# Optimization experiments

Measured on AMD Instinct MI355X. Metric: run time of the kernel, lower is better.

Reference implementation:

```python
import jax, jax.numpy as jnp
from jax import lax
import numpy as np

C = 256       # residual_channels == skip_channels
B = 4
T = 4096
LATENT = 128
NB = 4        # n_blocks
NL = 10       # n_layers
ENC_DILS = tuple(2 ** i for i in range(NL)) * NB   # 40 encoder blocks
DEC_DILS = tuple(2 ** i for i in range(NL))        # 10 decoder blocks


def causal_conv(x, W, b, d):
    # x: [B, Cin, T], W: [Cout, Cin, k], left-pad by (k-1)*d for causality
    pad = (W.shape[-1] - 1) * d
    y = lax.conv_general_dilated(x, W, (1,), [(pad, 0)], rhs_dilation=(d,),
                                 dimension_numbers=('NCH', 'OIH', 'NCH'))
    return y + b[None, :, None]


def gated_block(h, Wf, bf, Wg, bg, Wr, br, Ws, bs, d):
    f = jnp.tanh(causal_conv(h, Wf, bf, d))
    g = jax.nn.sigmoid(causal_conv(h, Wg, bg, d))
    out = f * g
    res = jnp.einsum('oc,bct->bot', Wr, out) + br[None, :, None] + h
    skip = jnp.einsum('oc,bct->bot', Ws, out) + bs[None, :, None]
    return res, skip


def setup_inputs() -> dict:
    key = jax.random.key(0)
    ks = jax.random.split(key, 24)
    s = 0.05
    nE = NB * NL
    d = {}
    d['x'] = jax.random.normal(ks[0], (B, 1, T), jnp.float32)
    d['eps'] = jax.random.normal(ks[1], (B, LATENT), jnp.float32)
    d['enc_in_W'] = jax.random.normal(ks[2], (C, 1, 2)) * s
    d['enc_in_b'] = jnp.zeros((C,), jnp.float32)
    d['enc_Wf'] = jax.random.normal(ks[3], (nE, C, C, 2)) * s
    d['enc_bf'] = jnp.zeros((nE, C), jnp.float32)
    d['enc_Wg'] = jax.random.normal(ks[4], (nE, C, C, 2)) * s
    d['enc_bg'] = jnp.zeros((nE, C), jnp.float32)
    d['enc_Wr'] = jax.random.normal(ks[5], (nE, C, C)) * s
    d['enc_br'] = jnp.zeros((nE, C), jnp.float32)
    d['enc_Ws'] = jax.random.normal(ks[6], (nE, C, C)) * s
    d['enc_bs'] = jnp.zeros((nE, C), jnp.float32)
    d['fc_mu_W'] = jax.random.normal(ks[7], (LATENT, C)) * s
    d['fc_mu_b'] = jnp.zeros((LATENT,), jnp.float32)
    d['fc_lv_W'] = jax.random.normal(ks[8], (LATENT, C)) * s
    d['fc_lv_b'] = jnp.zeros((LATENT,), jnp.float32)
    d['dec_in_W'] = jax.random.normal(ks[9], (C, LATENT)) * s
    d['dec_in_b'] = jnp.zeros((C,), jnp.float32)
    d['dec_Wf'] = jax.random.normal(ks[10], (NL, C, C, 2)) * s
    d['dec_bf'] = jnp.zeros((NL, C), jnp.float32)
    d['dec_Wg'] = jax.random.normal(ks[11], (NL, C, C, 2)) * s
    d['dec_bg'] = jnp.zeros((NL, C), jnp.float32)
    d['dec_Wr'] = jax.random.normal(ks[12], (NL, C, C)) * s
    d['dec_br'] = jnp.zeros((NL, C), jnp.float32)
    d['out_W'] = jax.random.normal(ks[13], (1, C)) * s
    d['out_b'] = jnp.zeros((1,), jnp.float32)
    return d


def _forward(x, eps, enc_in_W, enc_in_b, enc_Wf, enc_bf, enc_Wg, enc_bg,
             enc_Wr, enc_br, enc_Ws, enc_bs, fc_mu_W, fc_mu_b, fc_lv_W, fc_lv_b,
             dec_in_W, dec_in_b, dec_Wf, dec_bf, dec_Wg, dec_bg, dec_Wr, dec_br,
             out_W, out_b):
    # --- encode ---
    h = causal_conv(x, enc_in_W, enc_in_b, 1)
    skip_sum = jnp.zeros((h.shape[0], C, h.shape[2]), h.dtype)
    for i, dil in enumerate(ENC_DILS):
        h, skip = gated_block(h, enc_Wf[i], enc_bf[i], enc_Wg[i], enc_bg[i],
                              enc_Wr[i], enc_br[i], enc_Ws[i], enc_bs[i], dil)
        skip_sum = skip_sum + skip
    pooled = skip_sum.mean(axis=-1)                      # [B, C]
    mu = pooled @ fc_mu_W.T + fc_mu_b                    # [B, LATENT]
    logvar = pooled @ fc_lv_W.T + fc_lv_b
    # --- reparameterize ---
    z = mu + eps * jnp.exp(0.5 * logvar)
    # --- decode (length-1 sequence) ---
    h2 = (jnp.einsum('ol,bl->bo', dec_in_W, z) + dec_in_b)[:, :, None]  # [B, C, 1]
    for i, dil in enumerate(DEC_DILS):
        f = jnp.tanh(causal_conv(h2, dec_Wf[i], dec_bf[i], dil))
        g = jax.nn.sigmoid(causal_conv(h2, dec_Wg[i], dec_bg[i], dil))
        out = f * g
        h2 = jnp.einsum('oc,bct->bot', dec_Wr[i], out) + dec_br[i][None, :, None] + h2
    y = jnp.einsum('oc,bct->bot', out_W, h2) + out_b[None, :, None]     # [B, 1, 1]
    return (y, mu, logvar)


def reference(x, eps, enc_in_W, enc_in_b, enc_Wf, enc_bf, enc_Wg, enc_bg,
              enc_Wr, enc_br, enc_Ws, enc_bs, fc_mu_W, fc_mu_b, fc_lv_W, fc_lv_b,
              dec_in_W, dec_in_b, dec_Wf, dec_bf, dec_Wg, dec_bg, dec_Wr, dec_br,
              out_W, out_b):
    return _forward(x, eps, enc_in_W, enc_in_b, enc_Wf, enc_bf, enc_Wg, enc_bg,
                    enc_Wr, enc_br, enc_Ws, enc_bs, fc_mu_W, fc_mu_b, fc_lv_W, fc_lv_b,
                    dec_in_W, dec_in_b, dec_Wf, dec_bf, dec_Wg, dec_bg, dec_Wr, dec_br,
                    out_W, out_b)
```

## Files before the change

### kernel.cpp

```cpp
#include <hip/hip_runtime.h>

typedef unsigned short u16;
typedef __attribute__((ext_vector_type(8))) __bf16 bf16x8;
typedef __attribute__((ext_vector_type(4))) float f32x4;

constexpr int C = 256;
constexpr int T = 4096;
constexpr int B = 4;
constexpr int NENC = 40;
constexpr int NDEC = 10;
constexpr int TILE = 64;

__device__ __forceinline__ float bf2f(u16 v) {
  union { unsigned u; float f; } x;
  x.u = ((unsigned)v) << 16;
  return x.f;
}
__device__ __forceinline__ u16 f2bf(float f) {
  union { float ff; unsigned u; } x;
  x.ff = f;
  unsigned r = x.u + 0x7fffu + ((x.u >> 16) & 1u);
  return (u16)(r >> 16);
}
__device__ __forceinline__ int swz(int row, int col) {
  int g = ((row & 7) ^ (row >> 3)) & 7;
  return row * 512 + (col ^ (g << 3));
}

typedef __attribute__((address_space(1))) const unsigned int* gp1_t;
typedef __attribute__((address_space(3))) unsigned int* lp3_t;
__device__ __forceinline__ void gl_lds16(const u16* g, u16* l) {
  __builtin_amdgcn_global_load_lds((gp1_t)(const void*)g, (lp3_t)(void*)l, 16, 0, 0);
}

__global__ void k_pack1(const float* __restrict__ Wf, const float* __restrict__ Wg,
                        u16* __restrict__ penc1, int total) {
  int p = blockIdx.x * 256 + threadIdx.x;
  if (p >= total) return;
  int lane = p & 63;
  int s = (p >> 6) & 3;
  int c = (p >> 8) & 15;
  int wv = (p >> 12) & 7;
  int layer = p >> 15;
  int co = wv * 32 + (s & 1) * 16 + (lane & 15);
  int k = c * 32 + (lane >> 4) * 8;
  const float* src = (s >= 2 ? Wg : Wf) + ((size_t)layer * C + co) * 512 + k;
  u16* dst = penc1 + (size_t)p * 8;
#pragma unroll
  for (int r = 0; r < 8; ++r) dst[r] = f2bf(src[r]);
}

__global__ void k_pack2(const float* __restrict__ Wr, u16* __restrict__ penc2, int total) {
  int p = blockIdx.x * 256 + threadIdx.x;
  if (p >= total) return;
  int lane = p & 63;
  int s = (p >> 6) & 1;
  int c = (p >> 7) & 7;
  int wv = (p >> 10) & 7;
  int layer = p >> 13;
  int co = wv * 32 + s * 16 + (lane & 15);
  int k = c * 32 + (lane >> 4) * 8;
  const float* src = Wr + ((size_t)layer * C + co) * 256 + k;
  u16* dst = penc2 + (size_t)p * 8;
#pragma unroll
  for (int r = 0; r < 8; ++r) dst[r] = f2bf(src[r]);
}

__global__ void k_packd(const float* __restrict__ dWf, const float* __restrict__ dWg,
                        const float* __restrict__ dWr, const float* __restrict__ dinW,
                        u16* __restrict__ pdfg, u16* __restrict__ pdr,
                        u16* __restrict__ tdin) {
  int p = blockIdx.x * 256 + threadIdx.x;
  if (p < 163840) {
    int lane = p & 63;
    int s = (p >> 6) & 1;
    int c = (p >> 7) & 7;
    int wv = (p >> 10) & 15;
    int layer = p >> 14;
    int co = wv * 16 + (lane & 15);
    int k = c * 32 + (lane >> 4) * 8;
    const float* src = (s ? dWg : dWf) + (((size_t)(layer * C + co)) * C + k) * 2 + 1;
    u16* dst = pdfg + (size_t)p * 8;
#pragma unroll
    for (int r = 0; r < 8; ++r) dst[r] = f2bf(src[2 * r]);
  } else if (p < 245760) {
    int q = p - 163840;
    int lane = q & 63;
    int c = (q >> 6) & 7;
    int wv = (q >> 9) & 15;
    int layer = q >> 13;
    int co = wv * 16 + (lane & 15);
    int k = c * 32 + (lane >> 4) * 8;
    const float* src = dWr + ((size_t)(layer * C + co)) * C + k;
    u16* dst = pdr + (size_t)q * 8;
#pragma unroll
    for (int r = 0; r < 8; ++r) dst[r] = f2bf(src[r]);
  } else if (p < 249856) {
    int u = p - 245760;
#pragma unroll
    for (int r = 0; r < 8; ++r) tdin[u * 8 + r] = f2bf(dinW[u * 8 + r]);
  }
}

__global__ void k_zero(float* __restrict__ p, int n) {
  int i = blockIdx.x * 256 + threadIdx.x;
  if (i < n) p[i] = 0.f;
}

__global__ void k_input(const float* __restrict__ x, const float* __restrict__ W,
                        const float* __restrict__ bin, float* __restrict__ h) {
  int idx = blockIdx.x * 256 + threadIdx.x;
  int t = idx & (T - 1);
  int c = (idx >> 12) & (C - 1);
  int b = idx >> 20;
  float xv = x[b * T + t];
  float xp = (t > 0) ? x[b * T + t - 1] : 0.f;
  h[idx] = W[2 * c] * xp + W[2 * c + 1] * xv + bin[c];
}

__global__ __launch_bounds__(1024, 4) void k_enc(
    const float* __restrict__ hin, float* __restrict__ hout, float* __restrict__ rowsum_l,
    const u16* __restrict__ pw1, const float* __restrict__ bfb,
    const float* __restrict__ bgb,
    const u16* __restrict__ pw2, const float* __restrict__ brb,
    int dil) {
  extern __shared__ __align__(16) u16 smem[];
  const int tid = threadIdx.x;
  const int wave = tid >> 6;
  const int lane = tid & 63;
  const int ncol = lane & 15;
  const int quad = lane >> 4;
  const int wg = blockIdx.x;
  const int b = wg >> 6;
  const int t0 = (wg & 63) * TILE;
  const float* hb = hin + b * C * T;

  const int co0 = wave * 16;
  const int kq = quad * 8;
  const int off1 = (wg >> 3) & 15;
  const int off2 = (wg >> 3) & 7;
  const u16* b1w = pw1 + (wave >> 1) * 32768 + (wave & 1) * 512 + lane * 8;
  const u16* b2w = pw2 + (wave >> 1) * 8192 + (wave & 1) * 512 + lane * 8;

  const int n4 = tid & 15;
  const int cib = tid >> 4;
  float4 v0[4], v1[4];
  const bool al4 = ((dil & 3) == 0);
  if (t0 >= dil) {
#pragma unroll
    for (int j = 0; j < 4; ++j) {
      int ci = cib + j * 64;
      const float* p = hb + ci * T + t0 + n4 * 4 - dil;
      if (al4) {
        v0[j] = *(const float4*)p;
      } else {
        v0[j].x = p[0]; v0[j].y = p[1]; v0[j].z = p[2]; v0[j].w = p[3];
      }
      v1[j] = *(const float4*)(hb + ci * T + t0 + n4 * 4);
    }
  } else {
#pragma unroll
    for (int j = 0; j < 4; ++j) {
      int ci = cib + j * 64;
      int tb = t0 + n4 * 4 - dil;
      const float* p = hb + ci * T + tb;
      v0[j].x = (tb + 0 >= 0) ? p[0] : 0.f;
      v0[j].y = (tb + 1 >= 0) ? p[1] : 0.f;
      v0[j].z = (tb + 2 >= 0) ? p[2] : 0.f;
      v0[j].w = (tb + 3 >= 0) ? p[3] : 0.f;
      v1[j] = *(const float4*)(hb + ci * T + t0 + n4 * 4);
    }
  }
#pragma unroll
  for (int j = 0; j < 4; ++j) {
    int ci = cib + j * 64;
    const float* p0 = (const float*)&v0[j];
    const float* p1 = (const float*)&v1[j];
#pragma unroll
    for (int r = 0; r < 4; ++r) {
      unsigned w32 = (unsigned)f2bf(p0[r]) | ((unsigned)f2bf(p1[r]) << 16);
      *(unsigned*)(&smem[swz(n4 * 4 + r, 2 * ci)]) = w32;
    }
  }

  bf16x8 wf[2], wg_[2];
  {
    const u16* gs = b1w + (off1 & 15) * 2048;
    wf[0] = *(const bf16x8*)gs;
    wg_[0] = *(const bf16x8*)(gs + 1024);
  }
  __syncthreads();

  f32x4 acc[2][4];
#pragma unroll
  for (int m = 0; m < 2; ++m)
#pragma unroll
    for (int nt = 0; nt < 4; ++nt)
      acc[m][nt] = (f32x4){0.f, 0.f, 0.f, 0.f};

#pragma unroll 2
  for (int c = 0; c < 16; ++c) {
    const int cb = c & 1;
    if (c < 15) {
      const u16* gs = b1w + ((c + 1 + off1) & 15) * 2048;
      wf[cb ^ 1] = *(const bf16x8*)gs;
      wg_[cb ^ 1] = *(const bf16x8*)(gs + 1024);
    }
    const int kk = ((c + off1) & 15) * 32 + kq;
    bf16x8 bfr[4];
#pragma unroll
    for (int nt = 0; nt < 4; ++nt)
      bfr[nt] = *(const bf16x8*)(&smem[swz(nt * 16 + ncol, kk)]);
#pragma unroll
    for (int nt = 0; nt < 4; ++nt) {
      acc[0][nt] = __builtin_amdgcn_mfma_f32_16x16x32_bf16(wf[cb], bfr[nt], acc[0][nt], 0, 0, 0);
      acc[1][nt] = __builtin_amdgcn_mfma_f32_16x16x32_bf16(wg_[cb], bfr[nt], acc[1][nt], 0, 0, 0);
    }
  }

  bf16x8 w2[2];
  {
    const u16* gs = b2w + (off2 & 7) * 1024;
    w2[0] = *(const bf16x8*)gs;
  }
  __syncthreads();

  float* rsb = rowsum_l + b * C;
  {
    const int cob = co0 + quad * 4;
    float bfv[4], bgv[4], rs[4];
#pragma unroll
    for (int r = 0; r < 4; ++r) {
      bfv[r] = bfb[cob + r];
      bgv[r] = bgb[cob + r];
      rs[r] = 0.f;
    }
#pragma unroll
    for (int nt = 0; nt < 4; ++nt) {
      const int n = nt * 16 + ncol;
      u16 pk[4];
#pragma unroll
      for (int r = 0; r < 4; ++r) {
        float fv = acc[0][nt][r] + bfv[r];
        float gv = acc[1][nt][r] + bgv[r];
        float th = 1.f - 2.f / (__expf(2.f * fv) + 1.f);
        float sg = 1.f / (1.f + __expf(-gv));
        float o = th * sg;
        rs[r] += o;
        pk[r] = f2bf(o);
      }
      uint2 w;
      w.x = (unsigned)pk[0] | ((unsigned)pk[1] << 16);
      w.y = (unsigned)pk[2] | ((unsigned)pk[3] << 16);
      *(uint2*)(&smem[swz(n, cob)]) = w;
    }
#pragma unroll
    for (int r = 0; r < 4; ++r) {
      float s = rs[r];
      s += __shfl_xor(s, 1);
      s += __shfl_xor(s, 2);
      s += __shfl_xor(s, 4);
      s += __shfl_xor(s, 8);
      if (ncol == 0) atomicAdd(&rsb[cob + r], s);
    }
  }
  __syncthreads();

  f32x4 acc2[4];
#pragma unroll
  for (int nt = 0; nt < 4; ++nt)
    acc2[nt] = (f32x4){0.f, 0.f, 0.f, 0.f};

#pragma unroll 2
  for (int c = 0; c < 8; ++c) {
    const int cb = c & 1;
    if (c < 7) {
      const u16* gs = b2w + ((c + 1 + off2) & 7) * 1024;
      w2[cb ^ 1] = *(const bf16x8*)gs;
    }
    const int kk = ((c + off2) & 7) * 32 + kq;
    bf16x8 bfr[4];
#pragma unroll
    for (int nt = 0; nt < 4; ++nt)
      bfr[nt] = *(const bf16x8*)(&smem[swz(nt * 16 + ncol, kk)]);
#pragma unroll
    for (int nt = 0; nt < 4; ++nt)
      acc2[nt] = __builtin_amdgcn_mfma_f32_16x16x32_bf16(w2[cb], bfr[nt], acc2[nt], 0, 0, 0);
  }
  __syncthreads();

  float* fb = (float*)smem;
  {
    const int cob = co0 + quad * 4;
#pragma unroll
    for (int nt = 0; nt < 4; ++nt) {
      const int t = nt * 16 + ncol;
#pragma unroll
      for (int r = 0; r < 4; ++r)
        fb[(cob + r) * 66 + t] = acc2[nt][r] + brb[cob + r];
    }
  }
  __syncthreads();
  float* ho = hout + b * C * T;
#pragma unroll
  for (int j = 0; j < 4; ++j) {
    const int ci = cib + j * 64;
    const float* fr = fb + ci * 66 + n4 * 4;
    float4 o;
    o.x = fr[0] + v1[j].x;
    o.y = fr[1] + v1[j].y;
    o.z = fr[2] + v1[j].z;
    o.w = fr[3] + v1[j].w;
    *(float4*)(ho + ci * T + t0 + n4 * 4) = o;
  }
}

__global__ __launch_bounds__(256) void k_skip(
    const float* __restrict__ encWs, const float* __restrict__ encbs,
    const float* __restrict__ rowsum, float* __restrict__ pooled) {
  __shared__ float rs[B][C];
  const int l = blockIdx.x;
  const int co = threadIdx.x;
  for (int i = co; i < B * C; i += 256) rs[i >> 8][i & 255] = rowsum[l * B * C + i];
  __syncthreads();
  const float* Wrow = encWs + (size_t)l * C * C + co * C;
  float bs = encbs[l * C + co] * (float)T;
  float d[B] = {0.f, 0.f, 0.f, 0.f};
  for (int ci = 0; ci < C; ci += 4) {
    float4 w = *(const float4*)(Wrow + ci);
#pragma unroll
    for (int b = 0; b < B; ++b)
      d[b] += w.x * rs[b][ci] + w.y * rs[b][ci + 1] + w.z * rs[b][ci + 2] + w.w * rs[b][ci + 3];
  }
#pragma unroll
  for (int b = 0; b < B; ++b) atomicAdd(&pooled[b * C + co], d[b] + bs);
}

__global__ __launch_bounds__(256) void k_fc(
    const float* __restrict__ pooled,
    const float* __restrict__ muW, const float* __restrict__ mub,
    const float* __restrict__ lvW, const float* __restrict__ lvb,
    float* __restrict__ mlbuf, float* __restrict__ dout) {
  __shared__ float pm[B * C];
  const int tid = threadIdx.x;
  for (int i = tid; i < B * C; i += 256) pm[i] = pooled[i] * (1.f / (float)T);
  __syncthreads();
  const int waveG = blockIdx.x * 4 + (tid >> 6);
  const int lane = tid & 63;
  for (int j = 0; j < 16; ++j) {
    int d = waveG * 16 + j;
    int b = d >> 8, r = d & 255, which = r >> 7, l = r & 127;
    const float* Wrow = (which ? lvW : muW) + l * C;
    const float* p = pm + b * C;
    float s = Wrow[lane] * p[lane] + Wrow[lane + 64] * p[lane + 64] +
              Wrow[lane + 128] * p[lane + 128] + Wrow[lane + 192] * p[lane + 192];
#pragma unroll
    for (int off = 32; off; off >>= 1) s += __shfl_xor(s, off);
    if (lane == 0) {
      float val = s + (which ? lvb[l] : mub[l]);
      mlbuf[which * 512 + b * 128 + l] = val;
      dout[4 + which * 512 + b * 128 + l] = val;
    }
  }
}

__global__ __launch_bounds__(1024, 1) void k_dec(
    const float* __restrict__ mlbuf, const float* __restrict__ eps,
    const u16* __restrict__ tdin, const float* __restrict__ dinb,
    const u16* __restrict__ pdfg, const float* __restrict__ dbf,
    const float* __restrict__ dbg,
    const u16* __restrict__ pdr, const float* __restrict__ dbr,
    const float* __restrict__ outW, const float* __restrict__ outb,
    float* __restrict__ dout) {
  extern __shared__ __align__(16) u16 dsm[];
  __shared__ __align__(16) u16 Ah[16][264];
  __shared__ __align__(16) u16 Ao[16][264];
  __shared__ float h2f[4][256];
  __shared__ float outred[4];
  const int tid = threadIdx.x;
  const int wave = tid >> 6;
  const int lane = tid & 63;
  const int ncol = lane & 15;
  const int quad = lane >> 4;
  const int kq = quad * 8;
  const int co = wave * 16 + ncol;
  u16* wreg = dsm + wave * 4096;

  bf16x8 tdw[4];
  {
    const u16* wp = tdin + co * 128;
#pragma unroll
    for (int it = 0; it < 4; ++it) tdw[it] = *(const bf16x8*)(wp + it * 32 + kq);
  }

  if (tid < 512) {
    int b = tid >> 7, l = tid & 127;
    float mu = mlbuf[b * 128 + l];
    float lv = mlbuf[512 + b * 128 + l];
    Ah[b][l] = f2bf(mu + eps[b * 128 + l] * expf(0.5f * lv));
  }
  if (tid < 4) outred[tid] = 0.f;
  __syncthreads();

  {
    f32x4 acch = (f32x4){0.f, 0.f, 0.f, 0.f};
#pragma unroll
    for (int it = 0; it < 4; ++it) {
      bf16x8 af = *(const bf16x8*)(&Ah[ncol][it * 32 + kq]);
      acch = __builtin_amdgcn_mfma_f32_16x16x32_bf16(af, tdw[it], acch, 0, 0, 0);
    }
    __syncthreads();
    if (quad == 0) {
      float bias = dinb[co];
#pragma unroll
      for (int r = 0; r < 4; ++r) {
        float hv = acch[r] + bias;
        h2f[r][co] = hv;
        Ah[r][co] = f2bf(hv);
      }
    }
  }
  {
    const u16* fb = pdfg + wave * 8192 + lane * 8;
#pragma unroll
    for (int cc = 0; cc < 4; ++cc) {
      gl_lds16(fb + cc * 1024, wreg + cc * 1024);
      gl_lds16(fb + cc * 1024 + 512, wreg + cc * 1024 + 512);
    }
  }
  __syncthreads();

  for (int i = 0; i < NDEC; ++i) {
    const u16* fb = pdfg + (i * 16 + wave) * 8192 + lane * 8;
    const u16* rb = pdr + (i * 16 + wave) * 4096 + lane * 8;

    f32x4 accf = (f32x4){0.f, 0.f, 0.f, 0.f};
    f32x4 accg = (f32x4){0.f, 0.f, 0.f, 0.f};
#pragma unroll
    for (int c = 0; c < 8; ++c) {
      if (c == 4) asm volatile("s_waitcnt vmcnt(6)" ::: "memory");
      else if (c == 5) asm volatile("s_waitcnt vmcnt(4)" ::: "memory");
      else if (c == 6) asm volatile("s_waitcnt vmcnt(2)" ::: "memory");
      else if (c == 7) asm volatile("s_waitcnt vmcnt(0)" ::: "memory");
      const u16* bufp = wreg + (c & 3) * 1024;
      bf16x8 bf_ = *(const bf16x8*)(bufp + lane * 8);
      bf16x8 bg_ = *(const bf16x8*)(bufp + 512 + lane * 8);
      bf16x8 af = *(const bf16x8*)(&Ah[ncol][c * 32 + kq]);
      accf = __builtin_amdgcn_mfma_f32_16x16x32_bf16(af, bf_, accf, 0, 0, 0);
      accg = __builtin_amdgcn_mfma_f32_16x16x32_bf16(af, bg_, accg, 0, 0, 0);
      if (c < 4) {
        asm volatile("s_waitcnt lgkmcnt(0)" ::: "memory");
        gl_lds16(fb + (c + 4) * 1024, wreg + (c & 3) * 1024);
        gl_lds16(fb + (c + 4) * 1024 + 512, wreg + (c & 3) * 1024 + 512);
      }
    }
    asm volatile("s_waitcnt lgkmcnt(0)" ::: "memory");
#pragma unroll
    for (int cc = 0; cc < 4; ++cc) gl_lds16(rb + cc * 512, wreg + cc * 1024);

    if (quad == 0) {
      float bfv = dbf[i * C + co];
      float bgv = dbg[i * C + co];
#pragma unroll
      for (int r = 0; r < 4; ++r) {
        float fv = accf[r] + bfv;
        float gv = accg[r] + bgv;
        float th = 1.f - 2.f / (__expf(2.f * fv) + 1.f);
        float sg = 1.f / (1.f + __expf(-gv));
        Ao[r][co] = f2bf(th * sg);
      }
    }
    __syncthreads();

    f32x4 accr = (f32x4){0.f, 0.f, 0.f, 0.f};
#pragma unroll
    for (int c = 0; c < 8; ++c) {
      if (c == 4) asm volatile("s_waitcnt vmcnt(3)" ::: "memory");
      else if (c == 5) asm volatile("s_waitcnt vmcnt(2)" ::: "memory");
      else if (c == 6) asm volatile("s_waitcnt vmcnt(1)" ::: "memory");
      else if (c == 7) asm volatile("s_waitcnt vmcnt(0)" ::: "memory");
      bf16x8 br_ = *(const bf16x8*)(wreg + (c & 3) * 1024 + lane * 8);
      bf16x8 af = *(const bf16x8*)(&Ao[ncol][c * 32 + kq]);
      accr = __builtin_amdgcn_mfma_f32_16x16x32_bf16(af, br_, accr, 0, 0, 0);
      if (c < 4) {
        asm volatile("s_waitcnt lgkmcnt(0)" ::: "memory");
        gl_lds16(rb + (c + 4) * 512, wreg + (c & 3) * 1024);
      }
    }
    if (i + 1 < NDEC) {
      const u16* nfb = pdfg + ((i + 1) * 16 + wave) * 8192 + lane * 8;
      asm volatile("s_waitcnt lgkmcnt(0)" ::: "memory");
#pragma unroll
      for (int cc = 0; cc < 4; ++cc) {
        gl_lds16(nfb + cc * 1024, wreg + cc * 1024);
        gl_lds16(nfb + cc * 1024 + 512, wreg + cc * 1024 + 512);
      }
    }
    if (quad == 0) {
      float brv = dbr[i * C + co];
#pragma unroll
      for (int r = 0; r < 4; ++r) {
        float hv = h2f[r][co] + accr[r] + brv;
        h2f[r][co] = hv;
        Ah[r][co] = f2bf(hv);
      }
    }
    __syncthreads();
  }

  {
    int b = tid >> 8, c = tid & 255;
    float val = outW[c] * h2f[b][c];
#pragma unroll
    for (int off = 32; off; off >>= 1) val += __shfl_xor(val, off);
    if (lane == 0) atomicAdd(&outred[b], val);
  }
  __syncthreads();
  if (tid < 4) dout[tid] = outred[tid] + outb[0];
}

extern "C" void kernel_launch(void* const* d_in, const int* in_sizes, int n_in,
                              void* d_out, int out_size, void* d_ws, size_t ws_size,
                              hipStream_t stream) {
  const float* x      = (const float*)d_in[0];
  const float* eps    = (const float*)d_in[1];
  const float* encinW = (const float*)d_in[2];
  const float* encinb = (const float*)d_in[3];
  const float* encWf  = (const float*)d_in[4];
  const float* encbf  = (const float*)d_in[5];
  const float* encWg  = (const float*)d_in[6];
  const float* encbg  = (const float*)d_in[7];
  const float* encWr  = (const float*)d_in[8];
  const float* encbr  = (const float*)d_in[9];
  const float* encWs  = (const float*)d_in[10];
  const float* encbs  = (const float*)d_in[11];
  const float* muW    = (const float*)d_in[12];
  const float* mub    = (const float*)d_in[13];
  const float* lvW    = (const float*)d_in[14];
  const float* lvb    = (const float*)d_in[15];
  const float* dinW   = (const float*)d_in[16];
  const float* dinb   = (const float*)d_in[17];
  const float* dWf    = (const float*)d_in[18];
  const float* dbf    = (const float*)d_in[19];
  const float* dWg    = (const float*)d_in[20];
  const float* dbg    = (const float*)d_in[21];
  const float* dWr    = (const float*)d_in[22];
  const float* dbr    = (const float*)d_in[23];
  const float* outW   = (const float*)d_in[24];
  const float* outb   = (const float*)d_in[25];
  float* dout = (float*)d_out;

  char* ws = (char*)d_ws;
  float* hA = (float*)ws;
  float* hB = hA + (size_t)B * C * T;
  float* pooled = hB + (size_t)B * C * T;
  float* mlbuf = pooled + B * C;
  float* rowsum = mlbuf + 1024;
  u16* penc1 = (u16*)(rowsum + NENC * B * C);
  u16* penc2 = penc1 + (size_t)10485760;
  u16* pdfg = penc2 + (size_t)2621440;
  u16* pdr = pdfg + (size_t)1310720;
  u16* tdin = pdr + (size_t)655360;

  (void)hipFuncSetAttribute(reinterpret_cast<const void*>(k_enc),
                            hipFuncAttributeMaxDynamicSharedMemorySize, 67584);
  (void)hipFuncSetAttribute(reinterpret_cast<const void*>(k_dec),
                            hipFuncAttributeMaxDynamicSharedMemorySize, 131072);

  k_pack1<<<(1310720 + 255) / 256, 256, 0, stream>>>(encWf, encWg, penc1, 1310720);
  k_pack2<<<(327680 + 255) / 256, 256, 0, stream>>>(encWr, penc2, 327680);
  k_packd<<<(249856 + 255) / 256, 256, 0, stream>>>(dWf, dWg, dWr, dinW, pdfg, pdr, tdin);

  const int nZ = B * C + 1024 + NENC * B * C;
  k_zero<<<(nZ + 255) / 256, 256, 0, stream>>>(pooled, nZ);
  k_input<<<(B * C * T) / 256, 256, 0, stream>>>(x, encinW, encinb, hA);

  for (int i = 0; i < NENC; ++i) {
    const int dil = 1 << (i % 10);
    const float* hi = (i & 1) ? hB : hA;
    float* ho = (i & 1) ? hA : hB;
    k_enc<<<256, 1024, 67584, stream>>>(
        hi, ho, rowsum + (size_t)i * B * C,
        penc1 + (size_t)i * 262144, encbf + (size_t)i * C,
        encbg + (size_t)i * C,
        penc2 + (size_t)i * 65536, encbr + (size_t)i * C,
        dil);
  }

  k_skip<<<NENC, 256, 0, stream>>>(encWs, encbs, rowsum, pooled);
  k_fc<<<16, 256, 0, stream>>>(pooled, muW, mub, lvW, lvb, mlbuf, dout);
  k_dec<<<1, 1024, 131072, stream>>>(mlbuf, eps, tdin, dinb, pdfg, dbf, dbg,
                                     pdr, dbr, outW, outb, dout);
}
```

Baseline: 1.395 ms.

## Halve encoder time tile and double workgroups with 8 waves each covering 32 channels

The encoder block kernel now processes 32 time steps per workgroup instead of 64, launching 512 workgroups of 512 threads rather than 256 of 1024. Each wave computes a 32-output-channel slab with four weight fragments per k-step over two time subtiles, and shared memory is halved. The intent is to fill more CUs on the 256-CU GPU and cut per-workgroup latency. In exchange each weight fragment is reused across fewer time columns, so total weight traffic from L2 doubles.

Result: slower. 1.745 ms (+25.1%).

```diff
diff --git a/kernel.cpp b/kernel.cpp
--- a/kernel.cpp
+++ b/kernel.cpp
@@ -9,7 +9,7 @@
 constexpr int B = 4;
 constexpr int NENC = 40;
 constexpr int NDEC = 10;
-constexpr int TILE = 64;
+constexpr int TILE = 32;
 
 __device__ __forceinline__ float bf2f(u16 v) {
   union { unsigned u; float f; } x;
@@ -118,7 +118,7 @@
   h[idx] = W[2 * c] * xp + W[2 * c + 1] * xv + bin[c];
 }
 
-__global__ __launch_bounds__(1024, 4) void k_enc(
+__global__ __launch_bounds__(512, 4) void k_enc(
     const float* __restrict__ hin, float* __restrict__ hout, float* __restrict__ rowsum_l,
     const u16* __restrict__ pw1, const float* __restrict__ bfb,
     const float* __restrict__ bgb,
@@ -131,19 +131,19 @@
   const int ncol = lane & 15;
   const int quad = lane >> 4;
   const int wg = blockIdx.x;
-  const int b = wg >> 6;
-  const int t0 = (wg & 63) * TILE;
+  const int b = wg >> 7;
+  const int t0 = (wg & 127) * TILE;
   const float* hb = hin + b * C * T;
 
-  const int co0 = wave * 16;
+  const int co0 = wave * 32;
   const int kq = quad * 8;
   const int off1 = (wg >> 3) & 15;
   const int off2 = (wg >> 3) & 7;
-  const u16* b1w = pw1 + (wave >> 1) * 32768 + (wave & 1) * 512 + lane * 8;
-  const u16* b2w = pw2 + (wave >> 1) * 8192 + (wave & 1) * 512 + lane * 8;
-
-  const int n4 = tid & 15;
-  const int cib = tid >> 4;
+  const u16* b1w = pw1 + wave * 32768 + lane * 8;
+  const u16* b2w = pw2 + wave * 8192 + lane * 8;
+
+  const int n4 = tid & 7;
+  const int cib = tid >> 3;
   float4 v0[4], v1[4];
   const bool al4 = ((dil & 3) == 0);
   if (t0 >= dil) {
@@ -183,19 +183,19 @@
     }
   }
 
-  bf16x8 wf[2], wg_[2];
+  bf16x8 wA[2][4];
   {
     const u16* gs = b1w + (off1 & 15) * 2048;
-    wf[0] = *(const bf16x8*)gs;
-    wg_[0] = *(const bf16x8*)(gs + 1024);
-  }
-  __syncthreads();
-
-  f32x4 acc[2][4];
-#pragma unroll
-  for (int m = 0; m < 2; ++m)
-#pragma unroll
-    for (int nt = 0; nt < 4; ++nt)
+#pragma unroll
+    for (int s = 0; s < 4; ++s) wA[0][s] = *(const bf16x8*)(gs + s * 512);
+  }
+  __syncthreads();
+
+  f32x4 acc[4][2];
+#pragma unroll
+  for (int m = 0; m < 4; ++m)
+#pragma unroll
+    for (int nt = 0; nt < 2; ++nt)
       acc[m][nt] = (f32x4){0.f, 0.f, 0.f, 0.f};
 
 #pragma unroll 2
@@ -203,31 +203,35 @@
     const int cb = c & 1;
     if (c < 15) {
       const u16* gs = b1w + ((c + 1 + off1) & 15) * 2048;
-      wf[cb ^ 1] = *(const bf16x8*)gs;
-      wg_[cb ^ 1] = *(const bf16x8*)(gs + 1024);
+#pragma unroll
+      for (int s = 0; s < 4; ++s) wA[cb ^ 1][s] = *(const bf16x8*)(gs + s * 512);
     }
     const int kk = ((c + off1) & 15) * 32 + kq;
-    bf16x8 bfr[4];
-#pragma unroll
-    for (int nt = 0; nt < 4; ++nt)
+    bf16x8 bfr[2];
+#pragma unroll
+    for (int nt = 0; nt < 2; ++nt)
       bfr[nt] = *(const bf16x8*)(&smem[swz(nt * 16 + ncol, kk)]);
 #pragma unroll
-    for (int nt = 0; nt < 4; ++nt) {
-      acc[0][nt] = __builtin_amdgcn_mfma_f32_16x16x32_bf16(wf[cb], bfr[nt], acc[0][nt], 0, 0, 0);
-      acc[1][nt] = __builtin_amdgcn_mfma_f32_16x16x32_bf16(wg_[cb], bfr[nt], acc[1][nt], 0, 0, 0);
-    }
-  }
-
-  bf16x8 w2[2];
+    for (int nt = 0; nt < 2; ++nt) {
+      acc[0][nt] = __builtin_amdgcn_mfma_f32_16x16x32_bf16(wA[cb][0], bfr[nt], acc[0][nt], 0, 0, 0);
+      acc[1][nt] = __builtin_amdgcn_mfma_f32_16x16x32_bf16(wA[cb][1], bfr[nt], acc[1][nt], 0, 0, 0);
+      acc[2][nt] = __builtin_amdgcn_mfma_f32_16x16x32_bf16(wA[cb][2], bfr[nt], acc[2][nt], 0, 0, 0);
+      acc[3][nt] = __builtin_amdgcn_mfma_f32_16x16x32_bf16(wA[cb][3], bfr[nt], acc[3][nt], 0, 0, 0);
+    }
+  }
+
+  bf16x8 wB[2][2];
   {
     const u16* gs = b2w + (off2 & 7) * 1024;
-    w2[0] = *(const bf16x8*)gs;
+    wB[0][0] = *(const bf16x8*)gs;
+    wB[0][1] = *(const bf16x8*)(gs + 512);
   }
   __syncthreads();
 
   float* rsb = rowsum_l + b * C;
-  {
-    const int cob = co0 + quad * 4;
+#pragma unroll
+  for (int j = 0; j < 2; ++j) {
+    const int cob = co0 + j * 16 + quad * 4;
     float bfv[4], bgv[4], rs[4];
 #pragma unroll
     for (int r = 0; r < 4; ++r) {
@@ -236,13 +240,13 @@
       rs[r] = 0.f;
     }
 #pragma unroll
-    for (int nt = 0; nt < 4; ++nt) {
+    for (int nt = 0; nt < 2; ++nt) {
       const int n = nt * 16 + ncol;
       u16 pk[4];
 #pragma unroll
       for (int r = 0; r < 4; ++r) {
-        float fv = acc[0][nt][r] + bfv[r];
-        float gv = acc[1][nt][r] + bgv[r];
+        float fv = acc[j][nt][r] + bfv[r];
+        float gv = acc[2 + j][nt][r] + bgv[r];
         float th = 1.f - 2.f / (__expf(2.f * fv) + 1.f);
         float sg = 1.f / (1.f + __expf(-gv));
         float o = th * sg;
@@ -266,38 +270,44 @@
   }
   __syncthreads();
 
-  f32x4 acc2[4];
-#pragma unroll
-  for (int nt = 0; nt < 4; ++nt)
-    acc2[nt] = (f32x4){0.f, 0.f, 0.f, 0.f};
+  f32x4 acc2[2][2];
+#pragma unroll
+  for (int m = 0; m < 2; ++m)
+#pragma unroll
+    for (int nt = 0; nt < 2; ++nt)
+      acc2[m][nt] = (f32x4){0.f, 0.f, 0.f, 0.f};
 
 #pragma unroll 2
   for (int c = 0; c < 8; ++c) {
     const int cb = c & 1;
     if (c < 7) {
       const u16* gs = b2w + ((c + 1 + off2) & 7) * 1024;
-      w2[cb ^ 1] = *(const bf16x8*)gs;
+      wB[cb ^ 1][0] = *(const bf16x8*)gs;
+      wB[cb ^ 1][1] = *(const bf16x8*)(gs + 512);
     }
     const int kk = ((c + off2) & 7) * 32 + kq;
-    bf16x8 bfr[4];
-#pragma unroll
-    for (int nt = 0; nt < 4; ++nt)
+    bf16x8 bfr[2];
+#pragma unroll
+    for (int nt = 0; nt < 2; ++nt)
       bfr[nt] = *(const bf16x8*)(&smem[swz(nt * 16 + ncol, kk)]);
 #pragma unroll
-    for (int nt = 0; nt < 4; ++nt)
-      acc2[nt] = __builtin_amdgcn_mfma_f32_16x16x32_bf16(w2[cb], bfr[nt], acc2[nt], 0, 0, 0);
+    for (int nt = 0; nt < 2; ++nt) {
+      acc2[0][nt] = __builtin_amdgcn_mfma_f32_16x16x32_bf16(wB[cb][0], bfr[nt], acc2[0][nt], 0, 0, 0);
+      acc2[1][nt] = __builtin_amdgcn_mfma_f32_16x16x32_bf16(wB[cb][1], bfr[nt], acc2[1][nt], 0, 0, 0);
+    }
   }
   __syncthreads();
 
   float* fb = (float*)smem;
-  {
-    const int cob = co0 + quad * 4;
-#pragma unroll
-    for (int nt = 0; nt < 4; ++nt) {
+#pragma unroll
+  for (int m = 0; m < 2; ++m) {
+    const int cob = co0 + m * 16 + quad * 4;
+#pragma unroll
+    for (int nt = 0; nt < 2; ++nt) {
       const int t = nt * 16 + ncol;
 #pragma unroll
       for (int r = 0; r < 4; ++r)
-        fb[(cob + r) * 66 + t] = acc2[nt][r] + brb[cob + r];
+        fb[(cob + r) * 34 + t] = acc2[m][nt][r] + brb[cob + r];
     }
   }
   __syncthreads();
@@ -305,7 +315,7 @@
 #pragma unroll
   for (int j = 0; j < 4; ++j) {
     const int ci = cib + j * 64;
-    const float* fr = fb + ci * 66 + n4 * 4;
+    const float* fr = fb + ci * 34 + n4 * 4;
     float4 o;
     o.x = fr[0] + v1[j].x;
     o.y = fr[1] + v1[j].y;
@@ -563,7 +573,7 @@
   u16* tdin = pdr + (size_t)655360;
 
   (void)hipFuncSetAttribute(reinterpret_cast<const void*>(k_enc),
-                            hipFuncAttributeMaxDynamicSharedMemorySize, 67584);
+                            hipFuncAttributeMaxDynamicSharedMemorySize, 34816);
   (void)hipFuncSetAttribute(reinterpret_cast<const void*>(k_dec),
                             hipFuncAttributeMaxDynamicSharedMemorySize, 131072);
 
@@ -579,7 +589,7 @@
     const int dil = 1 << (i % 10);
     const float* hi = (i & 1) ? hB : hA;
     float* ho = (i & 1) ? hA : hB;
-    k_enc<<<256, 1024, 67584, stream>>>(
+    k_enc<<<512, 512, 34816, stream>>>(
         hi, ho, rowsum + (size_t)i * B * C,
         penc1 + (size_t)i * 262144, encbf + (size_t)i * C,
         encbg + (size_t)i * C,
```
